# Kernel optimization log

Measured on AMD Instinct MI355X. Metric: run time of the kernel, lower is better.

Reference implementation:

```python
import jax, jax.numpy as jnp
import numpy as np

LC_A = 0.5887
LC_B = 0.2574
LC_WEIGHT = 0.0001
B, P, NPRACT, NPROB = 2048, 8192, 64, 1000


def setup_inputs() -> dict:
    key = jax.random.key(0)
    k1, k2, k3, k4, k5 = jax.random.split(key, 5)
    pred = jax.random.normal(k1, (B, P, 1), dtype=jnp.float32)
    labels = (jax.random.uniform(k2, (B, P)) < 0.5).astype(jnp.float32)
    scores = jax.random.randint(k3, (B, P), 0, 2, dtype=jnp.int32)
    problems = jax.random.randint(k4, (B, P), 0, NPROB, dtype=jnp.int32)
    practicing_problems = jnp.arange(NPRACT, dtype=jnp.int32)
    first = (jax.random.uniform(k5, (B, P)) < 0.5).astype(jnp.float32)
    return {"pred": pred, "labels": labels, "scores": scores,
            "problems": problems, "practicing_problems": practicing_problems,
            "first": first}


def reference(pred, labels, scores, problems, practicing_problems, first):
    pred_sq = pred[..., 0]                      # [B,P] logits
    mask = (scores == 1).astype(pred_sq.dtype)  # train-mode gather mask
    # BCEWithLogits, numerically stable, mean over gathered elems then /count again (as in source)
    bce = jnp.maximum(pred_sq, 0.0) - pred_sq * labels + jnp.log1p(jnp.exp(-jnp.abs(pred_sq)))
    cnt = jnp.sum(mask)
    labeled_loss = jnp.sum(bce * mask) / cnt / cnt
    # membership mask: problems in practicing_problems (sorted searchsorted, no [B,P,K] blowup)
    sp = jnp.sort(practicing_problems)
    idx = jnp.clip(jnp.searchsorted(sp, problems), 0, sp.shape[0] - 1)
    lc_mask = (sp[idx] == problems).astype(pred_sq.dtype)
    prediction = pred_sq * lc_mask * first      # [B,P]
    # zeros2end: stable argsort on zero-mask compacts nonzeros to row front
    order = jnp.argsort(prediction == 0, axis=1)
    comp = jnp.take_along_axis(prediction, order, axis=1)
    nz = comp != 0
    col_counts = jnp.sum(nz, axis=0)            # [P] students with an i-th nonzero attempt
    col_means = jnp.sum(comp, axis=0) / jnp.maximum(col_counts, 1).astype(comp.dtype)
    fitting_lc = LC_A * jnp.arange(1, P + 1, dtype=comp.dtype) ** (-LC_B)
    terms = jnp.where(col_counts > 0, (1.0 - col_means - fitting_lc) ** 2, 0.0)
    lc_loss = jnp.sum(terms)
    total_loss = (1.0 - LC_WEIGHT) * labeled_loss + LC_WEIGHT * jnp.sqrt(lc_loss)
    return total_loss
```

## Files before the change

kernel.cpp:

```cpp
#include <hip/hip_runtime.h>
#include <math.h>

#define P_DIM   8192
#define TB      1024
#define EPT     8
#define NWAVE   (TB / 64)
#define RCHUNKS 64

#define LC_A 0.5887f
#define LC_B 0.2574f
#define LC_W 0.0001

__global__ __launch_bounds__(TB, 8) void row_kernel(
    const float* __restrict__ pred, const float* __restrict__ labels,
    const int*   __restrict__ scores, const int* __restrict__ problems,
    const int*   __restrict__ pract, int npract,
    const float* __restrict__ first,
    float* __restrict__ bce_part, unsigned* __restrict__ cnt_part,
    float* __restrict__ staging, int W, unsigned* __restrict__ nnz,
    float* __restrict__ colsum, unsigned* __restrict__ colcnt)
{
    __shared__ unsigned bitmap[32];
    __shared__ int      sp[64];
    __shared__ int      hasBig;
    __shared__ unsigned waveTot[NWAVE];
    __shared__ float    redF[NWAVE];
    __shared__ unsigned redU[NWAVE];

    const int t    = threadIdx.x;
    const int lane = t & 63;
    const int wid  = t >> 6;
    const int b    = blockIdx.x;
    const int np   = npract < 64 ? npract : 64;

    const size_t base = (size_t)b * P_DIM + (size_t)t * EPT;

    const float4 p0 = *(const float4*)(pred     + base);
    const float4 p1 = *(const float4*)(pred     + base + 4);
    const float4 l0 = *(const float4*)(labels   + base);
    const float4 l1 = *(const float4*)(labels   + base + 4);
    const int4   s0 = *(const int4*)  (scores   + base);
    const int4   s1 = *(const int4*)  (scores   + base + 4);
    const int4   q0 = *(const int4*)  (problems + base);
    const int4   q1 = *(const int4*)  (problems + base + 4);
    const float4 f0 = *(const float4*)(first    + base);
    const float4 f1 = *(const float4*)(first    + base + 4);

    if (t < 32) bitmap[t] = 0;
    if (t == 0) hasBig = 0;
    __syncthreads();
    if (t < np) {
        const int id = pract[t];
        sp[t] = id;
        if ((unsigned)id < 1024u) atomicOr(&bitmap[id >> 5], 1u << (id & 31));
        else hasBig = 1;
    }

    const float px[8] = {p0.x,p0.y,p0.z,p0.w, p1.x,p1.y,p1.z,p1.w};
    const float lx[8] = {l0.x,l0.y,l0.z,l0.w, l1.x,l1.y,l1.z,l1.w};
    const int   sx[8] = {s0.x,s0.y,s0.z,s0.w, s1.x,s1.y,s1.z,s1.w};

    float    bce_acc = 0.f;
    unsigned cnt_acc = 0;
#pragma unroll
    for (int k = 0; k < 8; ++k) {
        const float x = px[k];
        if (sx[k] == 1) {
            bce_acc += fmaxf(x, 0.f) - x * lx[k] + __logf(1.f + __expf(-fabsf(x)));
            cnt_acc++;
        }
    }

    __syncthreads();
    const int hb = hasBig;

    const int   qx[8] = {q0.x,q0.y,q0.z,q0.w, q1.x,q1.y,q1.z,q1.w};
    const float fx[8] = {f0.x,f0.y,f0.z,f0.w, f1.x,f1.y,f1.z,f1.w};

    float    vals[8];
    unsigned flags = 0;
    unsigned n     = 0;
#pragma unroll
    for (int k = 0; k < 8; ++k) {
        const unsigned v = (unsigned)qx[k];
        bool mem = (v < 1024u) && ((bitmap[v >> 5] >> (v & 31)) & 1u);
        if (hb && !mem) {
            for (int i = 0; i < np; ++i) mem |= (sp[i] == (int)v);
        }
        const float val = mem ? px[k] * fx[k] : 0.f;
        vals[k] = val;
        if (val != 0.f) { flags |= (1u << k); ++n; }
    }

    unsigned incl = n;
#pragma unroll
    for (int d = 1; d < 64; d <<= 1) {
        const unsigned u = __shfl_up(incl, d, 64);
        if (lane >= d) incl += u;
    }
    if (lane == 63) waveTot[wid] = incl;
    __syncthreads();
    unsigned woff = 0;
#pragma unroll
    for (int w = 0; w < NWAVE; ++w)
        if (w < wid) woff += waveTot[w];

    unsigned rank = woff + (incl - n);
    float* myrow = staging + (size_t)b * W;
#pragma unroll
    for (int k = 0; k < 8; ++k) {
        if (flags & (1u << k)) {
            if (rank < (unsigned)W) myrow[rank] = vals[k];
            else {
                atomicAdd(&colsum[rank], vals[k]);
                atomicAdd(&colcnt[rank], 1u);
            }
            ++rank;
        }
    }
    if (t == TB - 1) nnz[b] = woff + incl;

    for (int d = 32; d > 0; d >>= 1) {
        bce_acc += __shfl_down(bce_acc, d, 64);
        cnt_acc += __shfl_down(cnt_acc, d, 64);
    }
    if (lane == 0) { redF[wid] = bce_acc; redU[wid] = cnt_acc; }
    __syncthreads();
    if (t == 0) {
        float fb = 0.f; unsigned cu = 0;
        for (int w = 0; w < NWAVE; ++w) { fb += redF[w]; cu += redU[w]; }
        bce_part[b] = fb;
        cnt_part[b] = cu;
    }
}

__global__ __launch_bounds__(1024) void col_reduce(
    const float* __restrict__ staging, int W,
    const unsigned* __restrict__ nnz, int B, int rows_per_chunk,
    float* __restrict__ colsum, unsigned* __restrict__ colcnt)
{
    const int j  = threadIdx.x;
    const int r0 = blockIdx.x * rows_per_chunk;
    int r1 = r0 + rows_per_chunk; if (r1 > B) r1 = B;

    float s = 0.f; unsigned c = 0;
    for (int r = r0; r < r1; ++r) {
        const unsigned nz = nnz[r];
        if ((unsigned)j < nz) { s += staging[(size_t)r * W + j]; ++c; }
    }
    if (c) { atomicAdd(&colsum[j], s); atomicAdd(&colcnt[j], c); }
}

__global__ __launch_bounds__(1024) void final_kernel(
    const float* __restrict__ colsum, const unsigned* __restrict__ colcnt,
    const float* __restrict__ bce_part, const unsigned* __restrict__ cnt_part,
    int B, float* __restrict__ out)
{
    __shared__ double   redD[16];
    __shared__ float    redF[16];
    __shared__ unsigned redU[16];

    const int t = threadIdx.x, lane = t & 63, wid = t >> 6;

    double acc = 0.0;
    for (int j = t; j < P_DIM; j += 1024) {
        const unsigned c = colcnt[j];
        if (c) {
            const float fit = LC_A * powf((float)(j + 1), -LC_B);
            const float d   = 1.f - colsum[j] / (float)c - fit;
            acc += (double)d * (double)d;
        }
    }
    float    fb = 0.f;
    unsigned cu = 0;
    for (int i = t; i < B; i += 1024) { fb += bce_part[i]; cu += cnt_part[i]; }

    for (int d = 32; d > 0; d >>= 1) {
        acc += __shfl_down(acc, d, 64);
        fb  += __shfl_down(fb,  d, 64);
        cu  += __shfl_down(cu,  d, 64);
    }
    if (lane == 0) { redD[wid] = acc; redF[wid] = fb; redU[wid] = cu; }
    __syncthreads();
    if (t == 0) {
        double lc = 0.0, bs = 0.0; unsigned cnt = 0;
        for (int w = 0; w < 16; ++w) { lc += redD[w]; bs += (double)redF[w]; cnt += redU[w]; }
        const double c = (double)cnt;
        const double labeled = bs / c / c;
        out[0] = (float)((1.0 - LC_W) * labeled + LC_W * sqrt(lc));
    }
}

extern "C" void kernel_launch(void* const* d_in, const int* in_sizes, int n_in,
                              void* d_out, int out_size, void* d_ws, size_t ws_size,
                              hipStream_t stream)
{
    const float* pred     = (const float*)d_in[0];
    const float* labels   = (const float*)d_in[1];
    const int*   scores   = (const int*)  d_in[2];
    const int*   problems = (const int*)  d_in[3];
    const int*   pract    = (const int*)  d_in[4];
    const float* first    = (const float*)d_in[5];
    const int npract = in_sizes[4];
    const int B = in_sizes[1] / P_DIM;

    char* ws = (char*)d_ws;
    float*    colsum   = (float*)ws;
    unsigned* colcnt   = (unsigned*)(ws + (size_t)P_DIM * 4);
    float*    bce_part = (float*)(ws + (size_t)P_DIM * 8);
    unsigned* cnt_part = (unsigned*)(ws + (size_t)P_DIM * 8 + (size_t)B * 4);
    unsigned* nnz      = (unsigned*)(ws + (size_t)P_DIM * 8 + (size_t)B * 8);
    size_t off_stage   = ((size_t)P_DIM * 8 + (size_t)B * 12 + 255) & ~(size_t)255;
    float*    staging  = (float*)(ws + off_stage);

    size_t avail = ws_size > off_stage ? ws_size - off_stage : 0;
    size_t wmax  = avail / ((size_t)B * 4);
    int W = (int)(wmax > 512 ? 512 : (wmax & ~(size_t)63));
    if (W < 0) W = 0;

    hipMemsetAsync(d_ws, 0, (size_t)P_DIM * 8, stream);

    row_kernel<<<B, TB, 0, stream>>>(pred, labels, scores, problems,
                                     pract, npract, first,
                                     bce_part, cnt_part, staging, W, nnz,
                                     colsum, colcnt);
    if (W > 0) {
        const int rpc = (B + RCHUNKS - 1) / RCHUNKS;
        col_reduce<<<RCHUNKS, W, 0, stream>>>(staging, W, nnz, B, rpc,
                                              colsum, colcnt);
    }
    final_kernel<<<1, 1024, 0, stream>>>(colsum, colcnt, bce_part, cnt_part,
                                         B, (float*)d_out);
}
```

Baseline: 86.44 us.

## Split each row across four 256-thread blocks with per-segment compaction staging

```diff
diff --git a/kernel.cpp b/kernel.cpp
--- a/kernel.cpp
+++ b/kernel.cpp
@@ -2,38 +2,50 @@
 #include <math.h>
 
 #define P_DIM   8192
-#define TB      1024
+#define TB      256
 #define EPT     8
+#define SEG     (TB * EPT)
+#define NSEG    4
 #define NWAVE   (TB / 64)
 #define RCHUNKS 64
+#define MAXCOL  512
 
 #define LC_A 0.5887f
 #define LC_B 0.2574f
 #define LC_W 0.0001
+
+__global__ void bitmap_kernel(const int* __restrict__ pract, int npract,
+                              unsigned* __restrict__ bm, int* __restrict__ hasBig)
+{
+    const int t = threadIdx.x;
+    if (t < 32) bm[t] = 0;
+    if (t == 0) *hasBig = 0;
+    __syncthreads();
+    if (t < npract) {
+        const int id = pract[t];
+        if ((unsigned)id < 1024u) atomicOr(&bm[id >> 5], 1u << (id & 31));
+        else atomicExch(hasBig, 1);
+    }
+}
 
 __global__ __launch_bounds__(TB, 8) void row_kernel(
     const float* __restrict__ pred, const float* __restrict__ labels,
     const int*   __restrict__ scores, const int* __restrict__ problems,
     const int*   __restrict__ pract, int npract,
     const float* __restrict__ first,
+    const unsigned* __restrict__ bm, const int* __restrict__ hasBig,
     float* __restrict__ bce_part, unsigned* __restrict__ cnt_part,
-    float* __restrict__ staging, int W, unsigned* __restrict__ nnz,
-    float* __restrict__ colsum, unsigned* __restrict__ colcnt)
-{
-    __shared__ unsigned bitmap[32];
-    __shared__ int      sp[64];
-    __shared__ int      hasBig;
+    float* __restrict__ staging, int WQ, unsigned* __restrict__ qcnt,
+    uint2* __restrict__ ovf, unsigned* __restrict__ ovf_cnt, unsigned ovf_cap)
+{
     __shared__ unsigned waveTot[NWAVE];
-    __shared__ float    redF[NWAVE];
-    __shared__ unsigned redU[NWAVE];
 
     const int t    = threadIdx.x;
     const int lane = t & 63;
     const int wid  = t >> 6;
-    const int b    = blockIdx.x;
-    const int np   = npract < 64 ? npract : 64;
-
-    const size_t base = (size_t)b * P_DIM + (size_t)t * EPT;
+    const int blk  = blockIdx.x;
+    const size_t base = (size_t)(blk >> 2) * P_DIM + (size_t)(blk & 3) * SEG
+                      + (size_t)t * EPT;
 
     const float4 p0 = *(const float4*)(pred     + base);
     const float4 p1 = *(const float4*)(pred     + base + 4);
@@ -46,16 +58,6 @@
     const float4 f0 = *(const float4*)(first    + base);
     const float4 f1 = *(const float4*)(first    + base + 4);
 
-    if (t < 32) bitmap[t] = 0;
-    if (t == 0) hasBig = 0;
-    __syncthreads();
-    if (t < np) {
-        const int id = pract[t];
-        sp[t] = id;
-        if ((unsigned)id < 1024u) atomicOr(&bitmap[id >> 5], 1u << (id & 31));
-        else hasBig = 1;
-    }
-
     const float px[8] = {p0.x,p0.y,p0.z,p0.w, p1.x,p1.y,p1.z,p1.w};
     const float lx[8] = {l0.x,l0.y,l0.z,l0.w, l1.x,l1.y,l1.z,l1.w};
     const int   sx[8] = {s0.x,s0.y,s0.z,s0.w, s1.x,s1.y,s1.z,s1.w};
@@ -70,12 +72,18 @@
             cnt_acc++;
         }
     }
-
-    __syncthreads();
-    const int hb = hasBig;
+    for (int d = 32; d > 0; d >>= 1) {
+        bce_acc += __shfl_down(bce_acc, d, 64);
+        cnt_acc += __shfl_down(cnt_acc, d, 64);
+    }
+    if (lane == 0) {
+        bce_part[blk * NWAVE + wid] = bce_acc;
+        cnt_part[blk * NWAVE + wid] = cnt_acc;
+    }
 
     const int   qx[8] = {q0.x,q0.y,q0.z,q0.w, q1.x,q1.y,q1.z,q1.w};
     const float fx[8] = {f0.x,f0.y,f0.z,f0.w, f1.x,f1.y,f1.z,f1.w};
+    const int hb = *hasBig;
 
     float    vals[8];
     unsigned flags = 0;
@@ -83,9 +91,9 @@
 #pragma unroll
     for (int k = 0; k < 8; ++k) {
         const unsigned v = (unsigned)qx[k];
-        bool mem = (v < 1024u) && ((bitmap[v >> 5] >> (v & 31)) & 1u);
+        bool mem = (v < 1024u) && ((bm[v >> 5] >> (v & 31)) & 1u);
         if (hb && !mem) {
-            for (int i = 0; i < np; ++i) mem |= (sp[i] == (int)v);
+            for (int i = 0; i < npract; ++i) mem |= (pract[i] == (int)v);
         }
         const float val = mem ? px[k] * fx[k] : 0.f;
         vals[k] = val;
@@ -106,37 +114,29 @@
         if (w < wid) woff += waveTot[w];
 
     unsigned rank = woff + (incl - n);
-    float* myrow = staging + (size_t)b * W;
+    float* myrow = staging + (size_t)blk * WQ;
 #pragma unroll
     for (int k = 0; k < 8; ++k) {
         if (flags & (1u << k)) {
-            if (rank < (unsigned)W) myrow[rank] = vals[k];
+            if (rank < (unsigned)WQ) myrow[rank] = vals[k];
             else {
-                atomicAdd(&colsum[rank], vals[k]);
-                atomicAdd(&colcnt[rank], 1u);
+                const unsigned idx = atomicAdd(ovf_cnt, 1u);
+                if (idx < ovf_cap) {
+                    uint2 item;
+                    item.x = ((unsigned)blk << 11) | rank;
+                    item.y = __float_as_uint(vals[k]);
+                    ovf[idx] = item;
+                }
             }
             ++rank;
         }
     }
-    if (t == TB - 1) nnz[b] = woff + incl;
-
-    for (int d = 32; d > 0; d >>= 1) {
-        bce_acc += __shfl_down(bce_acc, d, 64);
-        cnt_acc += __shfl_down(cnt_acc, d, 64);
-    }
-    if (lane == 0) { redF[wid] = bce_acc; redU[wid] = cnt_acc; }
-    __syncthreads();
-    if (t == 0) {
-        float fb = 0.f; unsigned cu = 0;
-        for (int w = 0; w < NWAVE; ++w) { fb += redF[w]; cu += redU[w]; }
-        bce_part[b] = fb;
-        cnt_part[b] = cu;
-    }
-}
-
-__global__ __launch_bounds__(1024) void col_reduce(
-    const float* __restrict__ staging, int W,
-    const unsigned* __restrict__ nnz, int B, int rows_per_chunk,
+    if (t == TB - 1) qcnt[blk] = woff + incl;
+}
+
+__global__ __launch_bounds__(MAXCOL) void col_reduce(
+    const float* __restrict__ staging, int WQ,
+    const unsigned* __restrict__ qcnt, int B, int rows_per_chunk,
     float* __restrict__ colsum, unsigned* __restrict__ colcnt)
 {
     const int j  = threadIdx.x;
@@ -145,16 +145,67 @@
 
     float s = 0.f; unsigned c = 0;
     for (int r = r0; r < r1; ++r) {
-        const unsigned nz = nnz[r];
-        if ((unsigned)j < nz) { s += staging[(size_t)r * W + j]; ++c; }
+        const uint4 cc = *(const uint4*)(qcnt + (size_t)r * 4);
+        unsigned jj = (unsigned)j;
+        int      q  = -1;
+        unsigned lr = 0;
+        if (jj < cc.x) { q = 0; lr = jj; }
+        else { jj -= cc.x;
+            if (jj < cc.y) { q = 1; lr = jj; }
+            else { jj -= cc.y;
+                if (jj < cc.z) { q = 2; lr = jj; }
+                else { jj -= cc.z;
+                    if (jj < cc.w) { q = 3; lr = jj; }
+                }
+            }
+        }
+        if (q >= 0) {
+            ++c;
+            if (lr < (unsigned)WQ)
+                s += staging[((size_t)r * NSEG + q) * WQ + lr];
+        }
+        const unsigned total = cc.x + cc.y + cc.z + cc.w;
+        if (total > (unsigned)MAXCOL) {
+            for (unsigned j2 = (unsigned)MAXCOL + j; j2 < total; j2 += MAXCOL) {
+                unsigned u = j2; int q2; unsigned l2;
+                if (u < cc.x)      { q2 = 0; l2 = u; }
+                else if ((u -= cc.x) < cc.y) { q2 = 1; l2 = u; }
+                else if ((u -= cc.y) < cc.z) { q2 = 2; l2 = u; }
+                else               { q2 = 3; l2 = u - cc.z; }
+                atomicAdd(&colcnt[j2], 1u);
+                if (l2 < (unsigned)WQ)
+                    atomicAdd(&colsum[j2],
+                              staging[((size_t)r * NSEG + q2) * WQ + l2]);
+            }
+        }
     }
     if (c) { atomicAdd(&colsum[j], s); atomicAdd(&colcnt[j], c); }
+}
+
+__global__ void ovf_kernel(const uint2* __restrict__ ovf,
+                           const unsigned* __restrict__ ovf_cnt, unsigned ovf_cap,
+                           const unsigned* __restrict__ qcnt,
+                           float* __restrict__ colsum)
+{
+    unsigned nv = *ovf_cnt; if (nv > ovf_cap) nv = ovf_cap;
+    for (unsigned i = threadIdx.x; i < nv; i += blockDim.x) {
+        const uint2 item = ovf[i];
+        const unsigned blk = item.x >> 11;
+        const unsigned lr  = item.x & 2047u;
+        const unsigned r   = blk >> 2, q = blk & 3;
+        const uint4 cc = *(const uint4*)(qcnt + (size_t)r * 4);
+        unsigned col = lr;
+        if (q > 0) col += cc.x;
+        if (q > 1) col += cc.y;
+        if (q > 2) col += cc.z;
+        if (col < P_DIM) atomicAdd(&colsum[col], __uint_as_float(item.y));
+    }
 }
 
 __global__ __launch_bounds__(1024) void final_kernel(
     const float* __restrict__ colsum, const unsigned* __restrict__ colcnt,
     const float* __restrict__ bce_part, const unsigned* __restrict__ cnt_part,
-    int B, float* __restrict__ out)
+    int nparts, float* __restrict__ out)
 {
     __shared__ double   redD[16];
     __shared__ float    redF[16];
@@ -173,7 +224,7 @@
     }
     float    fb = 0.f;
     unsigned cu = 0;
-    for (int i = t; i < B; i += 1024) { fb += bce_part[i]; cu += cnt_part[i]; }
+    for (int i = t; i < nparts; i += 1024) { fb += bce_part[i]; cu += cnt_part[i]; }
 
     for (int d = 32; d > 0; d >>= 1) {
         acc += __shfl_down(acc, d, 64);
@@ -203,32 +254,49 @@
     const float* first    = (const float*)d_in[5];
     const int npract = in_sizes[4];
     const int B = in_sizes[1] / P_DIM;
+    const int nblk = B * NSEG;
 
     char* ws = (char*)d_ws;
     float*    colsum   = (float*)ws;
-    unsigned* colcnt   = (unsigned*)(ws + (size_t)P_DIM * 4);
-    float*    bce_part = (float*)(ws + (size_t)P_DIM * 8);
-    unsigned* cnt_part = (unsigned*)(ws + (size_t)P_DIM * 8 + (size_t)B * 4);
-    unsigned* nnz      = (unsigned*)(ws + (size_t)P_DIM * 8 + (size_t)B * 8);
-    size_t off_stage   = ((size_t)P_DIM * 8 + (size_t)B * 12 + 255) & ~(size_t)255;
-    float*    staging  = (float*)(ws + off_stage);
+    unsigned* colcnt   = (unsigned*)(ws + 32 * 1024);
+    unsigned* qcnt     = (unsigned*)(ws + 64 * 1024);
+    unsigned* ovf_cnt  = (unsigned*)(ws + 96 * 1024);
+    int*      hasBig   = (int*)     (ws + 96 * 1024 + 4);
+    unsigned* bm       = (unsigned*)(ws + 96 * 1024 + 128);
+    const size_t nparts = (size_t)nblk * NWAVE;
+    float*    bce_part = (float*)   (ws + 96 * 1024 + 256);
+    unsigned* cnt_part = (unsigned*)(ws + 96 * 1024 + 256 + nparts * 4);
+    size_t off_stage   = (96 * 1024 + 256 + nparts * 8 + 255) & ~(size_t)255;
 
     size_t avail = ws_size > off_stage ? ws_size - off_stage : 0;
-    size_t wmax  = avail / ((size_t)B * 4);
-    int W = (int)(wmax > 512 ? 512 : (wmax & ~(size_t)63));
-    if (W < 0) W = 0;
-
-    hipMemsetAsync(d_ws, 0, (size_t)P_DIM * 8, stream);
-
-    row_kernel<<<B, TB, 0, stream>>>(pred, labels, scores, problems,
-                                     pract, npract, first,
-                                     bce_part, cnt_part, staging, W, nnz,
-                                     colsum, colcnt);
-    if (W > 0) {
-        const int rpc = (B + RCHUNKS - 1) / RCHUNKS;
-        col_reduce<<<RCHUNKS, W, 0, stream>>>(staging, W, nnz, B, rpc,
-                                              colsum, colcnt);
-    }
+    int WQ = (int)(avail / ((size_t)nblk * 4));
+    if (WQ > 128) WQ = 128;
+    WQ &= ~31;
+    float* staging = (float*)(ws + off_stage);
+
+    size_t off_ovf = off_stage + (size_t)nblk * WQ * 4;
+    off_ovf = (off_ovf + 255) & ~(size_t)255;
+    unsigned ovf_cap = 0;
+    uint2* ovf = (uint2*)(ws + off_ovf);
+    if (ws_size > off_ovf + 8) ovf_cap = (unsigned)((ws_size - off_ovf) / 8);
+
+    hipMemsetAsync(ws, 0, 64 * 1024, stream);
+    hipMemsetAsync(ws + 96 * 1024, 0, 8, stream);
+
+    const int bt = npract <= 64 ? 64 : ((npract + 63) & ~63);
+    bitmap_kernel<<<1, bt, 0, stream>>>(pract, npract, bm, hasBig);
+
+    row_kernel<<<nblk, TB, 0, stream>>>(pred, labels, scores, problems,
+                                        pract, npract, first, bm, hasBig,
+                                        bce_part, cnt_part,
+                                        staging, WQ, qcnt,
+                                        ovf, ovf_cnt, ovf_cap);
+
+    const int rpc = (B + RCHUNKS - 1) / RCHUNKS;
+    col_reduce<<<RCHUNKS, MAXCOL, 0, stream>>>(staging, WQ, qcnt, B, rpc,
+                                               colsum, colcnt);
+    ovf_kernel<<<1, 256, 0, stream>>>(ovf, ovf_cnt, ovf_cap, qcnt, colsum);
+
     final_kernel<<<1, 1024, 0, stream>>>(colsum, colcnt, bce_part, cnt_part,
-                                         B, (float*)d_out);
-}
+                                         (int)nparts, (float*)d_out);
+}
```

New measurement: 112.6 us. +30.3%, slower.

## Process one row per wave with double-buffered global-to-LDS chunk loads

Applied to the files above, without the earlier changes.

```diff
diff --git a/kernel.cpp b/kernel.cpp
--- a/kernel.cpp
+++ b/kernel.cpp
@@ -2,151 +2,184 @@
 #include <math.h>
 
 #define P_DIM   8192
-#define TB      1024
-#define EPT     8
-#define NWAVE   (TB / 64)
+#define TB      256
+#define NWAVE   4
+#define CHUNK   512
+#define NCHUNK  (P_DIM / CHUNK)
 #define RCHUNKS 64
+#define WCAP    512
 
 #define LC_A 0.5887f
 #define LC_B 0.2574f
 #define LC_W 0.0001
 
-__global__ __launch_bounds__(TB, 8) void row_kernel(
+typedef float f32x4 __attribute__((ext_vector_type(4)));
+typedef int   i32x4 __attribute__((ext_vector_type(4)));
+
+__device__ __forceinline__ void load_lds16(const void* g, void* l) {
+    __builtin_amdgcn_global_load_lds(
+        (const __attribute__((address_space(1))) void*)g,
+        (__attribute__((address_space(3))) void*)l, 16, 0, 0);
+}
+
+__global__ __launch_bounds__(TB) void row_kernel(
     const float* __restrict__ pred, const float* __restrict__ labels,
     const int*   __restrict__ scores, const int* __restrict__ problems,
     const int*   __restrict__ pract, int npract,
     const float* __restrict__ first,
     float* __restrict__ bce_part, unsigned* __restrict__ cnt_part,
     float* __restrict__ staging, int W, unsigned* __restrict__ nnz,
-    float* __restrict__ colsum, unsigned* __restrict__ colcnt)
-{
-    __shared__ unsigned bitmap[32];
-    __shared__ int      sp[64];
-    __shared__ int      hasBig;
-    __shared__ unsigned waveTot[NWAVE];
-    __shared__ float    redF[NWAVE];
-    __shared__ unsigned redU[NWAVE];
-
-    const int t    = threadIdx.x;
-    const int lane = t & 63;
-    const int wid  = t >> 6;
-    const int b    = blockIdx.x;
-    const int np   = npract < 64 ? npract : 64;
-
-    const size_t base = (size_t)b * P_DIM + (size_t)t * EPT;
-
-    const float4 p0 = *(const float4*)(pred     + base);
-    const float4 p1 = *(const float4*)(pred     + base + 4);
-    const float4 l0 = *(const float4*)(labels   + base);
-    const float4 l1 = *(const float4*)(labels   + base + 4);
-    const int4   s0 = *(const int4*)  (scores   + base);
-    const int4   s1 = *(const int4*)  (scores   + base + 4);
-    const int4   q0 = *(const int4*)  (problems + base);
-    const int4   q1 = *(const int4*)  (problems + base + 4);
-    const float4 f0 = *(const float4*)(first    + base);
-    const float4 f1 = *(const float4*)(first    + base + 4);
-
-    if (t < 32) bitmap[t] = 0;
-    if (t == 0) hasBig = 0;
-    __syncthreads();
-    if (t < np) {
-        const int id = pract[t];
-        sp[t] = id;
-        if ((unsigned)id < 1024u) atomicOr(&bitmap[id >> 5], 1u << (id & 31));
-        else hasBig = 1;
-    }
-
-    const float px[8] = {p0.x,p0.y,p0.z,p0.w, p1.x,p1.y,p1.z,p1.w};
-    const float lx[8] = {l0.x,l0.y,l0.z,l0.w, l1.x,l1.y,l1.z,l1.w};
-    const int   sx[8] = {s0.x,s0.y,s0.z,s0.w, s1.x,s1.y,s1.z,s1.w};
+    float* __restrict__ colsum, int B)
+{
+    __shared__ __align__(16) float lds[NWAVE][2][5][CHUNK];
+
+    const int t = threadIdx.x, lane = t & 63, wid = t >> 6;
+    const int row = blockIdx.x * NWAVE + wid;
+    if (row >= B) return;
+    const size_t rowbase = (size_t)row * P_DIM;
+
+    const int np64 = npract < 64 ? npract : 64;
+    const int myid = (lane < np64) ? pract[lane] : -1;
+    const bool bigf = (lane < np64) && ((unsigned)myid >= 1024u);
+    const bool hb = (__ballot(bigf) != 0ull) || (npract > 64);
+
+    {
+        const int lo = lane * 4;
+#pragma unroll
+        for (int h = 0; h < 2; ++h) {
+            const int go = h * 256 + lo;
+            load_lds16(pred     + rowbase + go, &lds[wid][0][0][h * 256]);
+            load_lds16(labels   + rowbase + go, &lds[wid][0][1][h * 256]);
+            load_lds16(scores   + rowbase + go, &lds[wid][0][2][h * 256]);
+            load_lds16(problems + rowbase + go, &lds[wid][0][3][h * 256]);
+            load_lds16(first    + rowbase + go, &lds[wid][0][4][h * 256]);
+        }
+    }
+
+    unsigned bmreg = 0;
+    for (int j = 0; j < np64; ++j) {
+        const int idj = __shfl(myid, j, 64);
+        if ((unsigned)idj < 1024u && (int)((unsigned)idj >> 5) == lane)
+            bmreg |= 1u << (idj & 31);
+    }
 
     float    bce_acc = 0.f;
     unsigned cnt_acc = 0;
-#pragma unroll
-    for (int k = 0; k < 8; ++k) {
-        const float x = px[k];
-        if (sx[k] == 1) {
-            bce_acc += fmaxf(x, 0.f) - x * lx[k] + __logf(1.f + __expf(-fabsf(x)));
-            cnt_acc++;
-        }
-    }
-
-    __syncthreads();
-    const int hb = hasBig;
-
-    const int   qx[8] = {q0.x,q0.y,q0.z,q0.w, q1.x,q1.y,q1.z,q1.w};
-    const float fx[8] = {f0.x,f0.y,f0.z,f0.w, f1.x,f1.y,f1.z,f1.w};
-
-    float    vals[8];
-    unsigned flags = 0;
-    unsigned n     = 0;
-#pragma unroll
-    for (int k = 0; k < 8; ++k) {
-        const unsigned v = (unsigned)qx[k];
-        bool mem = (v < 1024u) && ((bitmap[v >> 5] >> (v & 31)) & 1u);
-        if (hb && !mem) {
-            for (int i = 0; i < np; ++i) mem |= (sp[i] == (int)v);
-        }
-        const float val = mem ? px[k] * fx[k] : 0.f;
-        vals[k] = val;
-        if (val != 0.f) { flags |= (1u << k); ++n; }
-    }
-
-    unsigned incl = n;
-#pragma unroll
-    for (int d = 1; d < 64; d <<= 1) {
-        const unsigned u = __shfl_up(incl, d, 64);
-        if (lane >= d) incl += u;
-    }
-    if (lane == 63) waveTot[wid] = incl;
-    __syncthreads();
-    unsigned woff = 0;
-#pragma unroll
-    for (int w = 0; w < NWAVE; ++w)
-        if (w < wid) woff += waveTot[w];
-
-    unsigned rank = woff + (incl - n);
-    float* myrow = staging + (size_t)b * W;
-#pragma unroll
-    for (int k = 0; k < 8; ++k) {
-        if (flags & (1u << k)) {
-            if (rank < (unsigned)W) myrow[rank] = vals[k];
-            else {
-                atomicAdd(&colsum[rank], vals[k]);
-                atomicAdd(&colcnt[rank], 1u);
+    unsigned rank    = 0;
+    float* myst = staging + (size_t)row * W;
+    int cur = 0;
+
+    for (int c = 0; c < NCHUNK; ++c) {
+        if (c + 1 < NCHUNK) {
+            const size_t nb = rowbase + (size_t)(c + 1) * CHUNK;
+            const int lo = lane * 4, nxt = cur ^ 1;
+#pragma unroll
+            for (int h = 0; h < 2; ++h) {
+                const int go = h * 256 + lo;
+                load_lds16(pred     + nb + go, &lds[wid][nxt][0][h * 256]);
+                load_lds16(labels   + nb + go, &lds[wid][nxt][1][h * 256]);
+                load_lds16(scores   + nb + go, &lds[wid][nxt][2][h * 256]);
+                load_lds16(problems + nb + go, &lds[wid][nxt][3][h * 256]);
+                load_lds16(first    + nb + go, &lds[wid][nxt][4][h * 256]);
             }
-            ++rank;
-        }
-    }
-    if (t == TB - 1) nnz[b] = woff + incl;
+            asm volatile("s_waitcnt vmcnt(10)" ::: "memory");
+        } else {
+            asm volatile("s_waitcnt vmcnt(0)" ::: "memory");
+        }
+        __builtin_amdgcn_sched_barrier(0);
+
+        float    vals[2][4];
+        unsigned fl[2], ncnt[2];
+#pragma unroll
+        for (int h = 0; h < 2; ++h) {
+            const int e = h * 256 + lane * 4;
+            const f32x4 p = *(const f32x4*)&lds[wid][cur][0][e];
+            const f32x4 l = *(const f32x4*)&lds[wid][cur][1][e];
+            const i32x4 s = *(const i32x4*)&lds[wid][cur][2][e];
+            const i32x4 q = *(const i32x4*)&lds[wid][cur][3][e];
+            const f32x4 f = *(const f32x4*)&lds[wid][cur][4][e];
+
+            unsigned fm = 0, n = 0;
+#pragma unroll
+            for (int k = 0; k < 4; ++k) {
+                const float x = p[k];
+                if (s[k] == 1) {
+                    bce_acc += fmaxf(x, 0.f) - x * l[k]
+                             + __logf(1.f + __expf(-fabsf(x)));
+                    cnt_acc++;
+                }
+                const unsigned v = (unsigned)q[k];
+                const unsigned word =
+                    (unsigned)__shfl((int)bmreg, (int)((v >> 5) & 63u), 64);
+                bool mem = (v < 1024u) && ((word >> (v & 31)) & 1u);
+                if (hb && !mem) {
+                    for (int ii = 0; ii < npract; ++ii)
+                        mem |= (pract[ii] == (int)v);
+                }
+                const float val = mem ? x * f[k] : 0.f;
+                vals[h][k] = val;
+                if (val != 0.f) { fm |= 1u << k; ++n; }
+            }
+            fl[h] = fm; ncnt[h] = n;
+        }
+
+        unsigned incl = ncnt[0] | (ncnt[1] << 9);
+#pragma unroll
+        for (int d = 1; d < 64; d <<= 1) {
+            const unsigned u = __shfl_up(incl, d, 64);
+            if (lane >= d) incl += u;
+        }
+        const unsigned tot  = (unsigned)__shfl((int)incl, 63, 64);
+        const unsigned tot0 = tot & 0x1ffu;
+        const unsigned ex0  = (incl & 0x1ffu) - ncnt[0];
+        const unsigned ex1  = (incl >> 9) - ncnt[1];
+
+        unsigned r0 = rank + ex0;
+        unsigned r1 = rank + tot0 + ex1;
+#pragma unroll
+        for (int h = 0; h < 2; ++h) {
+            unsigned r = h ? r1 : r0;
+            const unsigned fm = fl[h];
+#pragma unroll
+            for (int k = 0; k < 4; ++k) {
+                if (fm & (1u << k)) {
+                    if (r < (unsigned)W) myst[r] = vals[h][k];
+                    else if (r < (unsigned)P_DIM)
+                        atomicAdd(&colsum[r], vals[h][k]);
+                    ++r;
+                }
+            }
+        }
+        rank += tot0 + (tot >> 9);
+        cur ^= 1;
+    }
 
     for (int d = 32; d > 0; d >>= 1) {
         bce_acc += __shfl_down(bce_acc, d, 64);
         cnt_acc += __shfl_down(cnt_acc, d, 64);
     }
-    if (lane == 0) { redF[wid] = bce_acc; redU[wid] = cnt_acc; }
-    __syncthreads();
-    if (t == 0) {
-        float fb = 0.f; unsigned cu = 0;
-        for (int w = 0; w < NWAVE; ++w) { fb += redF[w]; cu += redU[w]; }
-        bce_part[b] = fb;
-        cnt_part[b] = cu;
-    }
-}
-
-__global__ __launch_bounds__(1024) void col_reduce(
-    const float* __restrict__ staging, int W,
-    const unsigned* __restrict__ nnz, int B, int rows_per_chunk,
-    float* __restrict__ colsum, unsigned* __restrict__ colcnt)
+    if (lane == 0) {
+        bce_part[row] = bce_acc;
+        cnt_part[row] = cnt_acc;
+        nnz[row]      = rank;
+    }
+}
+
+__global__ void col_reduce(const float* __restrict__ staging, int W,
+                           const unsigned* __restrict__ nnz, int B, int rpc,
+                           float* __restrict__ colsum,
+                           unsigned* __restrict__ colcnt)
 {
     const int j  = threadIdx.x;
-    const int r0 = blockIdx.x * rows_per_chunk;
-    int r1 = r0 + rows_per_chunk; if (r1 > B) r1 = B;
+    const int r0 = blockIdx.x * rpc;
+    int r1 = r0 + rpc; if (r1 > B) r1 = B;
 
     float s = 0.f; unsigned c = 0;
     for (int r = r0; r < r1; ++r) {
         const unsigned nz = nnz[r];
         if ((unsigned)j < nz) { s += staging[(size_t)r * W + j]; ++c; }
+        for (unsigned j2 = (unsigned)W + j; j2 < nz; j2 += (unsigned)W)
+            atomicAdd(&colcnt[j2], 1u);
     }
     if (c) { atomicAdd(&colsum[j], s); atomicAdd(&colcnt[j], c); }
 }
@@ -154,7 +187,7 @@
 __global__ __launch_bounds__(1024) void final_kernel(
     const float* __restrict__ colsum, const unsigned* __restrict__ colcnt,
     const float* __restrict__ bce_part, const unsigned* __restrict__ cnt_part,
-    int B, float* __restrict__ out)
+    int nparts, float* __restrict__ out)
 {
     __shared__ double   redD[16];
     __shared__ float    redF[16];
@@ -173,7 +206,7 @@
     }
     float    fb = 0.f;
     unsigned cu = 0;
-    for (int i = t; i < B; i += 1024) { fb += bce_part[i]; cu += cnt_part[i]; }
+    for (int i = t; i < nparts; i += 1024) { fb += bce_part[i]; cu += cnt_part[i]; }
 
     for (int d = 32; d > 0; d >>= 1) {
         acc += __shfl_down(acc, d, 64);
@@ -206,24 +239,26 @@
 
     char* ws = (char*)d_ws;
     float*    colsum   = (float*)ws;
-    unsigned* colcnt   = (unsigned*)(ws + (size_t)P_DIM * 4);
-    float*    bce_part = (float*)(ws + (size_t)P_DIM * 8);
-    unsigned* cnt_part = (unsigned*)(ws + (size_t)P_DIM * 8 + (size_t)B * 4);
-    unsigned* nnz      = (unsigned*)(ws + (size_t)P_DIM * 8 + (size_t)B * 8);
-    size_t off_stage   = ((size_t)P_DIM * 8 + (size_t)B * 12 + 255) & ~(size_t)255;
+    unsigned* colcnt   = (unsigned*)(ws + 32 * 1024);
+    unsigned* nnz      = (unsigned*)(ws + 64 * 1024);
+    float*    bce_part = (float*)   (ws + 64 * 1024 + (size_t)B * 4);
+    unsigned* cnt_part = (unsigned*)(ws + 64 * 1024 + (size_t)B * 8);
+    size_t off_stage   = (64 * 1024 + (size_t)B * 12 + 255) & ~(size_t)255;
     float*    staging  = (float*)(ws + off_stage);
 
     size_t avail = ws_size > off_stage ? ws_size - off_stage : 0;
-    size_t wmax  = avail / ((size_t)B * 4);
-    int W = (int)(wmax > 512 ? 512 : (wmax & ~(size_t)63));
-    if (W < 0) W = 0;
-
-    hipMemsetAsync(d_ws, 0, (size_t)P_DIM * 8, stream);
-
-    row_kernel<<<B, TB, 0, stream>>>(pred, labels, scores, problems,
-                                     pract, npract, first,
-                                     bce_part, cnt_part, staging, W, nnz,
-                                     colsum, colcnt);
+    int W = (int)(avail / ((size_t)B * 4));
+    if (W > WCAP) W = WCAP;
+    W &= ~63;
+
+    hipMemsetAsync(ws, 0, 64 * 1024, stream);
+
+    const int nblk = (B + NWAVE - 1) / NWAVE;
+    row_kernel<<<nblk, TB, 0, stream>>>(pred, labels, scores, problems,
+                                        pract, npract, first,
+                                        bce_part, cnt_part,
+                                        staging, W, nnz, colsum, B);
+
     if (W > 0) {
         const int rpc = (B + RCHUNKS - 1) / RCHUNKS;
         col_reduce<<<RCHUNKS, W, 0, stream>>>(staging, W, nnz, B, rpc,
```

Result: slower. 97.06 us (+12.3%).
